# Kernel tuning notes

Hardware: AMD Instinct MI355X
Metric: run time of the kernel (lower is better)

The kernel has to match this reference:

```python
import jax, jax.numpy as jnp
import numpy as np

IN_F = 4096
OUT_F = 11008
N_CLUSTERS = 16
TOPK = int(IN_F * 0.25)  # 1024


def setup_inputs() -> dict:
    key = jax.random.key(0)
    k1, k2, k3, k4 = jax.random.split(key, 4)
    x = jax.random.normal(k1, (1, 1, IN_F), jnp.float32)
    weight_full = jax.random.normal(k2, (OUT_F, IN_F), jnp.float32) * 0.02
    bias_full = jax.random.normal(k3, (OUT_F,), jnp.float32) * 0.02
    # cluster centers live in softmax-activation space (compared via cdist to a softmax)
    cluster_centers = jax.nn.softmax(
        jax.random.normal(k4, (N_CLUSTERS, IN_F), jnp.float32), axis=-1)
    return {"x": x, "weight_full": weight_full, "bias_full": bias_full,
            "cluster_centers": cluster_centers}


def reference(x, weight_full, bias_full, cluster_centers):
    # hot path: bsz * seq == 1
    x_flat = x.reshape(-1, x.shape[-1])                 # [1, in]
    x_avg = jnp.abs(jnp.mean(x_flat, axis=0))           # [in]
    activation = jax.nn.softmax(x_avg, axis=0)          # [in]
    # nearest cluster center (squared L2 has same argmin as L2)
    d2 = jnp.sum((cluster_centers - activation[None, :]) ** 2, axis=-1)  # [n_clusters]
    ci = jnp.argmin(d2)
    center = cluster_centers[ci]                        # [in]
    # per-cluster precomputed top-k column indices: argsort(center, descending)[:topk]
    _, topk_idx = jax.lax.top_k(center, TOPK)           # [topk]
    x_sel = jnp.take(x_flat, topk_idx, axis=1)          # [1, topk]
    w_sel = jnp.take(weight_full, topk_idx, axis=1)     # [out, topk]
    out = x_sel @ w_sel.T + bias_full                   # [1, out]
    return out.reshape(1, 1, -1)
```

## Files before the change

kernel.cpp:

```cpp
#include <hip/hip_runtime.h>

#define IN_F 4096
#define OUT_F 11008
#define NCLUST 16
#define TOPK 1024
#define NT 1024
#define NW 16
#define ROWS_PB 43

typedef float f4 __attribute__((ext_vector_type(4)));

__device__ __forceinline__ float dotf4(f4 a, f4 b) {
    return a[0] * b[0] + a[1] * b[1] + a[2] * b[2] + a[3] * b[3];
}
__device__ __forceinline__ float wredsum(float v) {
    for (int o = 32; o > 0; o >>= 1) v += __shfl_down(v, o, 64);
    return v;
}


__global__ __launch_bounds__(NT) void cluster_partials_kernel(
    const float* __restrict__ x,
    const float* __restrict__ centers,
    float* __restrict__ ws)
{
    const int tid  = threadIdx.x;
    const int lane = tid & 63;
    const int wid  = tid >> 6;
    const int b    = blockIdx.x;

    __shared__ float sdt[NW], scq[NW];

    f4 xv = ((const f4*)x)[tid];
    f4 ev;
    ev[0] = expf(fabsf(xv[0])); ev[1] = expf(fabsf(xv[1]));
    ev[2] = expf(fabsf(xv[2])); ev[3] = expf(fabsf(xv[3]));
    f4 cvv = ((const f4*)(centers + (size_t)b * IN_F))[tid];

    float dt = wredsum(dotf4(cvv, ev));
    float cq = wredsum(dotf4(cvv, cvv));
    if (lane == 0) { sdt[wid] = dt; scq[wid] = cq; }
    __syncthreads();
    if (tid == 0) {
        float D = 0.0f, Q = 0.0f;
        #pragma unroll
        for (int k = 0; k < NW; ++k) { D += sdt[k]; Q += scq[k]; }
        ws[IN_F + b]      = D;
        ws[IN_F + 16 + b] = Q;
    }
}

__global__ __launch_bounds__(NT) void finalize_mask_kernel(
    const float* __restrict__ x,
    const float* __restrict__ centers,
    float* __restrict__ ws)
{
    const int tid  = threadIdx.x;
    const int lane = tid & 63;
    const int wid  = tid >> 6;

    __shared__ unsigned int hist[NW * 256];
    __shared__ float swred[NW];
    __shared__ unsigned int wtot4[4], weq[NW];
    __shared__ unsigned int sprefix, sKrem, sG;
    __shared__ int sci;

    if (tid == 0) { sprefix = 0u; sKrem = TOPK; sG = 0u; }

    f4 xv = ((const f4*)x)[tid];
    {
        float e0 = expf(fabsf(xv[0])), e1 = expf(fabsf(xv[1]));
        float e2 = expf(fabsf(xv[2])), e3 = expf(fabsf(xv[3]));
        float s = wredsum(e0 + e1 + e2 + e3);
        if (lane == 0) swred[wid] = s;
        hist[tid] = 0u; hist[tid + 1024] = 0u;
        hist[tid + 2048] = 0u; hist[tid + 3072] = 0u;
    }
    __syncthreads();
    float S = 0.0f;
    #pragma unroll
    for (int k = 0; k < NW; ++k) S += swred[k];

    if (wid == 0) {
        float v = 3.0e38f;
        int bi = lane;
        if (lane < NCLUST)
            v = ws[IN_F + 16 + lane] - (2.0f / S) * ws[IN_F + lane];
        for (int off = 8; off > 0; off >>= 1) {
            float ov = __shfl_down(v, off, 64);
            int   oi = __shfl_down(bi, off, 64);
            if (ov < v) { v = ov; bi = oi; }
        }
        if (lane == 0) sci = bi;
    }
    __syncthreads();

    unsigned int cv[4];
    {
        f4 c = ((const f4*)(centers + (size_t)sci * IN_F))[tid];
        cv[0] = __float_as_uint(c[0]); cv[1] = __float_as_uint(c[1]);
        cv[2] = __float_as_uint(c[2]); cv[3] = __float_as_uint(c[3]);
    }

    for (int pass = 0; pass < 4; ++pass) {
        const int shift = 24 - 8 * pass;
        const unsigned int pfx  = sprefix;
        const unsigned int krem = sKrem;
        unsigned int* hp = &hist[wid * 256];
        #pragma unroll
        for (int j = 0; j < 4; ++j) {
            unsigned int u = cv[j];
            bool cand = (pass == 0) || ((u >> (shift + 8)) == pfx);
            if (cand) atomicAdd(&hp[(u >> shift) & 255u], 1u);
        }
        __syncthreads();
        unsigned int h = 0, s = 0;
        if (tid < 256) {
            #pragma unroll
            for (int w = 0; w < NW; ++w) { h += hist[w * 256 + tid]; hist[w * 256 + tid] = 0u; }
            s = h;
            for (int off = 1; off < 64; off <<= 1) {
                unsigned int v2 = __shfl_down(s, off, 64);
                if (lane + off < 64) s += v2;
            }
            if (lane == 0) wtot4[wid] = s;
        }
        __syncthreads();
        if (tid < 256) {
            unsigned int add = 0;
            #pragma unroll
            for (int w2 = 0; w2 < 4; ++w2) if (w2 > wid) add += wtot4[w2];
            unsigned int incl = s + add;
            unsigned int excl = incl - h;
            if (excl < krem && krem <= incl) {
                sprefix = (pfx << 8) | (unsigned int)tid;
                sKrem   = krem - excl;
            }
        }
        __syncthreads();
    }
    const unsigned int T = sprefix;

    unsigned int gt = 0, eq = 0;
    #pragma unroll
    for (int j = 0; j < 4; ++j) {
        gt += (cv[j] > T) ? 1u : 0u;
        eq += (cv[j] == T) ? 1u : 0u;
    }
    {
        unsigned int g = gt;
        for (int o = 32; o > 0; o >>= 1) g += __shfl_down(g, o, 64);
        if (lane == 0) atomicAdd(&sG, g);
    }
    unsigned int p = eq;
    for (int off = 1; off < 64; off <<= 1) {
        unsigned int v2 = __shfl_up(p, off, 64);
        if (lane >= off) p += v2;
    }
    if (lane == 63) weq[wid] = p;
    __syncthreads();
    unsigned int base = p - eq;
    #pragma unroll
    for (int w = 0; w < NW; ++w) if (w < wid) base += weq[w];
    const unsigned int needEq = TOPK - sG;

    {
        unsigned int r = 0;
        f4 o;
        o[0] = ((cv[0] > T) || ((cv[0] == T) && (base + r < needEq))) ? xv[0] : 0.0f; r += (cv[0] == T);
        o[1] = ((cv[1] > T) || ((cv[1] == T) && (base + r < needEq))) ? xv[1] : 0.0f; r += (cv[1] == T);
        o[2] = ((cv[2] > T) || ((cv[2] == T) && (base + r < needEq))) ? xv[2] : 0.0f; r += (cv[2] == T);
        o[3] = ((cv[3] > T) || ((cv[3] == T) && (base + r < needEq))) ? xv[3] : 0.0f;
        ((f4*)ws)[tid] = o;
    }
}

__global__ __launch_bounds__(NT) void matvec_kernel(
    const float* __restrict__ W,
    const float* __restrict__ xm,
    const float* __restrict__ bias,
    float* __restrict__ out)
{
    const int tid  = threadIdx.x;
    const int lane = tid & 63;
    const int wid  = tid >> 6;
    const int rbase = blockIdx.x * ROWS_PB;

    __shared__ float spart[ROWS_PB][NW + 1];

    const f4 xv = ((const f4*)xm)[tid];
    const f4* wp = (const f4*)(W + (size_t)rbase * IN_F);

    int r = 0;
    #pragma unroll 2
    for (; r + 4 <= ROWS_PB; r += 4) {
        f4 wa = __builtin_nontemporal_load(&wp[(size_t)(r + 0) * 1024 + tid]);
        f4 wb = __builtin_nontemporal_load(&wp[(size_t)(r + 1) * 1024 + tid]);
        f4 wc = __builtin_nontemporal_load(&wp[(size_t)(r + 2) * 1024 + tid]);
        f4 wd = __builtin_nontemporal_load(&wp[(size_t)(r + 3) * 1024 + tid]);
        float pa = dotf4(wa, xv);
        float pb = dotf4(wb, xv);
        float pc = dotf4(wc, xv);
        float pd = dotf4(wd, xv);
        #pragma unroll
        for (int o = 32; o > 0; o >>= 1) {
            pa += __shfl_down(pa, o, 64);
            pb += __shfl_down(pb, o, 64);
            pc += __shfl_down(pc, o, 64);
            pd += __shfl_down(pd, o, 64);
        }
        if (lane == 0) {
            spart[r + 0][wid] = pa;
            spart[r + 1][wid] = pb;
            spart[r + 2][wid] = pc;
            spart[r + 3][wid] = pd;
        }
    }
    for (; r < ROWS_PB; ++r) {
        f4 w = __builtin_nontemporal_load(&wp[(size_t)r * 1024 + tid]);
        float p = wredsum(dotf4(w, xv));
        if (lane == 0) spart[r][wid] = p;
    }
    __syncthreads();

    if (tid < ROWS_PB) {
        float s = 0.0f;
        #pragma unroll
        for (int w = 0; w < NW; ++w) s += spart[tid][w];
        const int row = rbase + tid;
        out[row] = s + bias[row];
    }
}

extern "C" void kernel_launch(void* const* d_in, const int* in_sizes, int n_in,
                              void* d_out, int out_size, void* d_ws, size_t ws_size,
                              hipStream_t stream) {
    const float* x       = (const float*)d_in[0];
    const float* weight  = (const float*)d_in[1];
    const float* bias    = (const float*)d_in[2];
    const float* centers = (const float*)d_in[3];
    float* out = (float*)d_out;
    float* ws  = (float*)d_ws;

    cluster_partials_kernel<<<NCLUST, NT, 0, stream>>>(x, centers, ws);
    finalize_mask_kernel<<<1, NT, 0, stream>>>(x, centers, ws);
    matvec_kernel<<<256, NT, 0, stream>>>(weight, ws, bias, out);
}
```

Before: 45.51 us.

## Fuse cluster partials and mask selection via last-block-done atomic counter

Merges the two preprocessing kernels into one 16-block kernel. Each block writes its partial distance terms, then bumps a global atomic counter, and the last block to finish runs the argmin, radix top-k threshold and mask write. This removes a kernel launch boundary at the cost of a memset launch to reset the counter. It also switches the weight loads in the matvec from nontemporal to ordinary loads, which changes cache behaviour for the streamed weights.

```diff
diff --git a/kernel.cpp b/kernel.cpp
--- a/kernel.cpp
+++ b/kernel.cpp
@@ -19,7 +19,7 @@
 }
 
 
-__global__ __launch_bounds__(NT) void cluster_partials_kernel(
+__global__ __launch_bounds__(NT) void select_mask_kernel(
     const float* __restrict__ x,
     const float* __restrict__ centers,
     float* __restrict__ ws)
@@ -29,63 +29,54 @@
     const int wid  = tid >> 6;
     const int b    = blockIdx.x;
 
-    __shared__ float sdt[NW], scq[NW];
+    __shared__ unsigned int hist[NW * 256];
+    __shared__ float swred[NW], sdt[NW], scq[NW];
+    __shared__ unsigned int wtot4[4], weq[NW];
+    __shared__ unsigned int sprefix, sKrem, sG;
+    __shared__ int sci, sfin;
+
+    unsigned int* done  = (unsigned int*)(ws + IN_F);
+    float* slot_dot = ws + IN_F + 8;
+    float* slot_csq = ws + IN_F + 24;
 
     f4 xv = ((const f4*)x)[tid];
     f4 ev;
     ev[0] = expf(fabsf(xv[0])); ev[1] = expf(fabsf(xv[1]));
     ev[2] = expf(fabsf(xv[2])); ev[3] = expf(fabsf(xv[3]));
     f4 cvv = ((const f4*)(centers + (size_t)b * IN_F))[tid];
-
-    float dt = wredsum(dotf4(cvv, ev));
-    float cq = wredsum(dotf4(cvv, cvv));
-    if (lane == 0) { sdt[wid] = dt; scq[wid] = cq; }
-    __syncthreads();
-    if (tid == 0) {
-        float D = 0.0f, Q = 0.0f;
-        #pragma unroll
-        for (int k = 0; k < NW; ++k) { D += sdt[k]; Q += scq[k]; }
-        ws[IN_F + b]      = D;
-        ws[IN_F + 16 + b] = Q;
-    }
-}
-
-__global__ __launch_bounds__(NT) void finalize_mask_kernel(
-    const float* __restrict__ x,
-    const float* __restrict__ centers,
-    float* __restrict__ ws)
-{
-    const int tid  = threadIdx.x;
-    const int lane = tid & 63;
-    const int wid  = tid >> 6;
-
-    __shared__ unsigned int hist[NW * 256];
-    __shared__ float swred[NW];
-    __shared__ unsigned int wtot4[4], weq[NW];
-    __shared__ unsigned int sprefix, sKrem, sG;
-    __shared__ int sci;
-
-    if (tid == 0) { sprefix = 0u; sKrem = TOPK; sG = 0u; }
-
-    f4 xv = ((const f4*)x)[tid];
-    {
-        float e0 = expf(fabsf(xv[0])), e1 = expf(fabsf(xv[1]));
-        float e2 = expf(fabsf(xv[2])), e3 = expf(fabsf(xv[3]));
-        float s = wredsum(e0 + e1 + e2 + e3);
-        if (lane == 0) swred[wid] = s;
+    {
+        float s  = wredsum(ev[0] + ev[1] + ev[2] + ev[3]);
+        float dt = wredsum(dotf4(cvv, ev));
+        float cq = wredsum(dotf4(cvv, cvv));
+        if (lane == 0) { swred[wid] = s; sdt[wid] = dt; scq[wid] = cq; }
+        if (tid == 0) { sprefix = 0u; sKrem = TOPK; sG = 0u; }
         hist[tid] = 0u; hist[tid + 1024] = 0u;
         hist[tid + 2048] = 0u; hist[tid + 3072] = 0u;
     }
     __syncthreads();
     float S = 0.0f;
-    #pragma unroll
-    for (int k = 0; k < NW; ++k) S += swred[k];
-
+    {
+        float D = 0.0f, Q = 0.0f;
+        #pragma unroll
+        for (int k = 0; k < NW; ++k) { S += swred[k]; D += sdt[k]; Q += scq[k]; }
+        if (tid == 0) {
+            slot_dot[b] = D;
+            slot_csq[b] = Q;
+            __threadfence();
+            unsigned int old = __hip_atomic_fetch_add(done, 1u, __ATOMIC_ACQ_REL,
+                                                      __HIP_MEMORY_SCOPE_AGENT);
+            sfin = (old == NCLUST - 1) ? 1 : 0;
+        }
+    }
+    __syncthreads();
+    if (!sfin) return;
+
+    __threadfence();
     if (wid == 0) {
         float v = 3.0e38f;
         int bi = lane;
         if (lane < NCLUST)
-            v = ws[IN_F + 16 + lane] - (2.0f / S) * ws[IN_F + lane];
+            v = slot_csq[lane] - (2.0f / S) * slot_dot[lane];
         for (int off = 8; off > 0; off >>= 1) {
             float ov = __shfl_down(v, off, 64);
             int   oi = __shfl_down(bi, off, 64);
@@ -194,10 +185,10 @@
     int r = 0;
     #pragma unroll 2
     for (; r + 4 <= ROWS_PB; r += 4) {
-        f4 wa = __builtin_nontemporal_load(&wp[(size_t)(r + 0) * 1024 + tid]);
-        f4 wb = __builtin_nontemporal_load(&wp[(size_t)(r + 1) * 1024 + tid]);
-        f4 wc = __builtin_nontemporal_load(&wp[(size_t)(r + 2) * 1024 + tid]);
-        f4 wd = __builtin_nontemporal_load(&wp[(size_t)(r + 3) * 1024 + tid]);
+        f4 wa = wp[(size_t)(r + 0) * 1024 + tid];
+        f4 wb = wp[(size_t)(r + 1) * 1024 + tid];
+        f4 wc = wp[(size_t)(r + 2) * 1024 + tid];
+        f4 wd = wp[(size_t)(r + 3) * 1024 + tid];
         float pa = dotf4(wa, xv);
         float pb = dotf4(wb, xv);
         float pc = dotf4(wc, xv);
@@ -217,7 +208,7 @@
         }
     }
     for (; r < ROWS_PB; ++r) {
-        f4 w = __builtin_nontemporal_load(&wp[(size_t)r * 1024 + tid]);
+        f4 w = wp[(size_t)r * 1024 + tid];
         float p = wredsum(dotf4(w, xv));
         if (lane == 0) spart[r][wid] = p;
     }
@@ -242,7 +233,7 @@
     float* out = (float*)d_out;
     float* ws  = (float*)d_ws;
 
-    cluster_partials_kernel<<<NCLUST, NT, 0, stream>>>(x, centers, ws);
-    finalize_mask_kernel<<<1, NT, 0, stream>>>(x, centers, ws);
+    hipMemsetAsync((void*)(ws + IN_F), 0, 4, stream);
+    select_mask_kernel<<<NCLUST, NT, 0, stream>>>(x, centers, ws);
     matvec_kernel<<<256, NT, 0, stream>>>(weight, ws, bias, out);
 }
```

Measured after the change: 50.47 us. 1.11x slower.
